# Optimization experiments

Hardware: AMD Instinct MI355X
Metric: run time of the kernel (lower is better)

Reference implementation:

```python
import jax, jax.numpy as jnp
import numpy as np

OUT_X = OUT_Y = OUT_Z = 12        # out_size
N_VOX = OUT_X * OUT_Y * OUT_Z
N_ROIS, N_PTS, C = 128, 160000, 64


def setup_inputs() -> dict:
    key = jax.random.key(0)
    k1, k2, k3, k4, k5, k6 = jax.random.split(key, 6)
    # rois: (N, 7) = [x, y, z_bottom, w(dx), l(dy), h(dz), ry]
    centers_xy = jax.random.uniform(k1, (N_ROIS, 2), minval=-40.0, maxval=40.0)
    z_bottom = jax.random.uniform(k2, (N_ROIS, 1), minval=-2.0, maxval=0.0)
    sizes = jax.random.uniform(k3, (N_ROIS, 3), minval=1.5, maxval=5.0)
    ry = jax.random.uniform(k4, (N_ROIS, 1), minval=-np.pi, maxval=np.pi)
    rois = jnp.concatenate([centers_xy, z_bottom, sizes, ry], axis=1).astype(jnp.float32)
    # points spread over the same scene extent so many fall inside rois
    pts = (jax.random.uniform(k5, (N_PTS, 3), minval=-1.0, maxval=1.0)
           * jnp.array([45.0, 45.0, 2.5], jnp.float32)).astype(jnp.float32)
    pts_feature = jax.random.normal(k6, (N_PTS, C), dtype=jnp.float32)
    return {"rois": rois, "pts": pts, "pts_feature": pts_feature}


def _voxel_segments(rois, pts):
    """Per (roi, point): flat voxel index in [0, N_VOX), or N_VOX if outside the roi."""
    cx, cy, cz, dx, dy, dz, rz = [rois[:, i:i + 1] for i in range(7)]  # (N,1)
    sx = pts[:, 0] - cx   # (N,P)
    sy = pts[:, 1] - cy
    sz = pts[:, 2] - cz   # z relative to box bottom
    cosa, sina = jnp.cos(-rz), jnp.sin(-rz)
    lx = sx * cosa - sy * sina  # rotate into roi-local frame
    ly = sx * sina + sy * cosa
    in_box = ((lx > -dx * 0.5) & (lx < dx * 0.5)
              & (ly > -dy * 0.5) & (ly < dy * 0.5)
              & (jnp.abs(sz - dz * 0.5) <= dz * 0.5))
    xi = jnp.clip(jnp.floor((lx + dx * 0.5) / (dx / OUT_X)), 0, OUT_X - 1).astype(jnp.int32)
    yi = jnp.clip(jnp.floor((ly + dy * 0.5) / (dy / OUT_Y)), 0, OUT_Y - 1).astype(jnp.int32)
    zi = jnp.clip(jnp.floor(sz / (dz / OUT_Z)), 0, OUT_Z - 1).astype(jnp.int32)
    seg = xi * (OUT_Y * OUT_Z) + yi * OUT_Z + zi
    return jnp.where(in_box, seg, N_VOX)  # (N, P) int32


def reference(rois, pts, pts_feature):
    seg = _voxel_segments(rois, pts)  # (N, P)
    ones = jnp.ones((pts.shape[0],), jnp.float32)

    def per_roi(s):
        mx = jax.ops.segment_max(pts_feature, s, num_segments=N_VOX + 1)[:N_VOX]  # (V, C)
        cnt = jax.ops.segment_sum(ones, s, num_segments=N_VOX + 1)[:N_VOX]        # (V,)
        return jnp.where(cnt[:, None] > 0, mx, 0.0)  # empty voxels -> 0, as in CUDA kernel

    pooled = jax.lax.map(per_roi, seg)  # (N, V, C); sequential over rois keeps memory bounded
    return pooled.reshape(N_ROIS, OUT_X, OUT_Y, OUT_Z, pts_feature.shape[-1])
```

## Files before the change

### kernel.cpp

```cpp
#include <hip/hip_runtime.h>

#define NROIS 128
#define OUTD  12
#define NVOX  (OUTD * OUTD * OUTD)
#define NCH   64
#define RPB   16
#define QCAP  1024

__device__ __forceinline__ unsigned enc_f32(float f) {
    unsigned b = __float_as_uint(f);
    return (b & 0x80000000u) ? ~b : (b | 0x80000000u);
}

__device__ __forceinline__ float dec_key(unsigned k) {
    unsigned b = (k & 0x80000000u) ? (k & 0x7fffffffu) : ~k;
    return __uint_as_float(b);
}

#define WS_REJ   0
#define WS_RAD2  (WS_REJ + NROIS * 16)
#define WS_FULL  (WS_RAD2 + NROIS * 4)

__global__ void roi_prep(const float* __restrict__ rois,
                         float4* __restrict__ rej, float* __restrict__ rad2,
                         float4* __restrict__ full)
{
    int r = threadIdx.x;
    if (r >= NROIS) return;
    float cx = rois[7 * r + 0];
    float cy = rois[7 * r + 1];
    float cz = rois[7 * r + 2];
    float dx = rois[7 * r + 3];
    float dy = rois[7 * r + 4];
    float dz = rois[7 * r + 5];
    float nrz = -rois[7 * r + 6];
    float ca = cosf(nrz), sa = sinf(nrz);
    float hx = __fmul_rn(dx, 0.5f);
    float hy = __fmul_rn(dy, 0.5f);
    float hz = __fmul_rn(dz, 0.5f);
    full[3 * r + 0] = make_float4(cx, cy, cz, ca);
    full[3 * r + 1] = make_float4(sa, hx, hy, hz);
    full[3 * r + 2] = make_float4(__fdiv_rn(dx, 12.0f), __fdiv_rn(dy, 12.0f),
                                  __fdiv_rn(dz, 12.0f), 0.0f);
    float R2 = 0.25f * (dx * dx + dy * dy);
    rad2[r] = R2 * 1.04f + 1e-4f;
    float zc = cz + hz;
    float zh = hz * 1.001f + 1e-3f;
    rej[r] = make_float4(cx, cy, zc, zh);
}

__global__ void __launch_bounds__(256) roi_pool_scatter(
        const float* __restrict__ pts,
        const float* __restrict__ feat,
        const float4* __restrict__ rej,
        const float* __restrict__ rad2,
        const float4* __restrict__ full,
        unsigned*    __restrict__ out,
        int npts)
{
    __shared__ float4   sRej[RPB];
    __shared__ float    sRad[RPB];
    __shared__ float4   sFull[RPB * 3];
    __shared__ unsigned sQp[QCAP];
    __shared__ unsigned sQk[QCAP];
    __shared__ unsigned sQn;

    int rbase = blockIdx.y * RPB;
    if (threadIdx.x == 0) sQn = 0;
    if (threadIdx.x < RPB) {
        sRej[threadIdx.x] = rej[rbase + threadIdx.x];
        sRad[threadIdx.x] = rad2[rbase + threadIdx.x];
    }
    if (threadIdx.x < RPB * 3)
        sFull[threadIdx.x] = full[rbase * 3 + threadIdx.x];
    __syncthreads();

    int p = blockIdx.x * blockDim.x + threadIdx.x;
    if (p < npts) {
        float px = pts[3 * p + 0];
        float py = pts[3 * p + 1];
        float pz = pts[3 * p + 2];

        for (int r = 0; r < RPB; ++r) {
            float4 q = sRej[r];
            float sx = px - q.x;
            float sy = py - q.y;
            float d2 = sx * sx + sy * sy;
            if (!((d2 < sRad[r]) && (fabsf(pz - q.z) <= q.w))) continue;

            float4 F0 = sFull[3 * r + 0];
            float4 F1 = sFull[3 * r + 1];
            float sz = __fsub_rn(pz, F0.z);
            float ca = F0.w, sa = F1.x;
            float hx = F1.y, hy = F1.z, hz = F1.w;
            float lx = __fsub_rn(__fmul_rn(sx, ca), __fmul_rn(sy, sa));
            float ly = __fadd_rn(__fmul_rn(sx, sa), __fmul_rn(sy, ca));

            bool in_box = (lx > -hx) && (lx < hx) &&
                          (ly > -hy) && (ly < hy) &&
                          (fabsf(__fsub_rn(sz, hz)) <= hz);
            if (!in_box) continue;

            float4 F2 = sFull[3 * r + 2];
            int xi = (int)floorf(__fdiv_rn(__fadd_rn(lx, hx), F2.x));
            int yi = (int)floorf(__fdiv_rn(__fadd_rn(ly, hy), F2.y));
            int zi = (int)floorf(__fdiv_rn(sz,                F2.z));
            xi = min(max(xi, 0), OUTD - 1);
            yi = min(max(yi, 0), OUTD - 1);
            zi = min(max(zi, 0), OUTD - 1);

            unsigned key = (unsigned)((rbase + r) * NVOX +
                                      xi * (OUTD * OUTD) + yi * OUTD + zi);

            unsigned idx = atomicAdd(&sQn, 1u);
            if (idx < QCAP) {
                sQp[idx] = (unsigned)p;
                sQk[idx] = key;
            } else {
                unsigned* dst = out + (size_t)key * NCH;
                const float* fp = feat + (size_t)p * NCH;
                #pragma unroll 1
                for (int c = 0; c < NCH; ++c)
                    atomicMax(dst + c, enc_f32(fp[c]));
            }
        }
    }

    __syncthreads();
    int nq   = min((int)sQn, QCAP);
    int wid  = threadIdx.x >> 6;
    int lane = threadIdx.x & 63;
    for (int i = wid; i < nq; i += 4) {
        unsigned pp = sQp[i];
        unsigned kk = sQk[i];
        float f = feat[(size_t)pp * NCH + lane];
        atomicMax(out + (size_t)kk * NCH + lane, enc_f32(f));
    }
}

__global__ void __launch_bounds__(256) decode_keys(unsigned* __restrict__ out, int n4)
{
    int i = blockIdx.x * blockDim.x + threadIdx.x;
    if (i >= n4) return;
    uint4 k = reinterpret_cast<uint4*>(out)[i];
    if ((k.x | k.y | k.z | k.w) == 0u) return;
    float4 f;
    f.x = (k.x == 0u) ? 0.0f : dec_key(k.x);
    f.y = (k.y == 0u) ? 0.0f : dec_key(k.y);
    f.z = (k.z == 0u) ? 0.0f : dec_key(k.z);
    f.w = (k.w == 0u) ? 0.0f : dec_key(k.w);
    reinterpret_cast<float4*>(out)[i] = f;
}

extern "C" void kernel_launch(void* const* d_in, const int* in_sizes, int n_in,
                              void* d_out, int out_size, void* d_ws, size_t ws_size,
                              hipStream_t stream)
{
    const float* rois = (const float*)d_in[0];
    const float* pts  = (const float*)d_in[1];
    const float* feat = (const float*)d_in[2];
    int npts = in_sizes[1] / 3;

    float4* rej  = (float4*)((char*)d_ws + WS_REJ);
    float*  rad2 = (float*)((char*)d_ws + WS_RAD2);
    float4* full = (float4*)((char*)d_ws + WS_FULL);

    hipMemsetAsync(d_out, 0, (size_t)out_size * sizeof(float), stream);

    roi_prep<<<1, NROIS, 0, stream>>>(rois, rej, rad2, full);

    dim3 grid((npts + 255) / 256, NROIS / RPB);
    roi_pool_scatter<<<grid, 256, 0, stream>>>(pts, feat, rej, rad2, full,
                                               (unsigned*)d_out, npts);

    int n4 = out_size / 4;
    decode_keys<<<(n4 + 255) / 256, 256, 0, stream>>>((unsigned*)d_out, n4);
}
```

Measured before the change: 120.9 us.

## Fuse ROI prep into scatter kernel and decode only touched voxels via bitmask

Removes the separate roi_prep launch by computing per-ROI parameters inside each scatter block's shared-memory setup. Adds a bitmask of touched voxel keys, set with atomicOr during scatter, so the decode pass visits only occupied voxels instead of streaming the whole output. This saves a kernel launch and a full read of the output buffer, at the cost of an extra memset, per-entry atomicOr traffic, and redundant trig per block.

```diff
diff --git a/kernel.cpp b/kernel.cpp
--- a/kernel.cpp
+++ b/kernel.cpp
@@ -4,6 +4,8 @@
 #define OUTD  12
 #define NVOX  (OUTD * OUTD * OUTD)
 #define NCH   64
+#define NKEYS (NROIS * NVOX)
+#define NWORDS (NKEYS / 32)
 #define RPB   16
 #define QCAP  1024
 
@@ -17,45 +19,12 @@
     return __uint_as_float(b);
 }
 
-#define WS_REJ   0
-#define WS_RAD2  (WS_REJ + NROIS * 16)
-#define WS_FULL  (WS_RAD2 + NROIS * 4)
-
-__global__ void roi_prep(const float* __restrict__ rois,
-                         float4* __restrict__ rej, float* __restrict__ rad2,
-                         float4* __restrict__ full)
-{
-    int r = threadIdx.x;
-    if (r >= NROIS) return;
-    float cx = rois[7 * r + 0];
-    float cy = rois[7 * r + 1];
-    float cz = rois[7 * r + 2];
-    float dx = rois[7 * r + 3];
-    float dy = rois[7 * r + 4];
-    float dz = rois[7 * r + 5];
-    float nrz = -rois[7 * r + 6];
-    float ca = cosf(nrz), sa = sinf(nrz);
-    float hx = __fmul_rn(dx, 0.5f);
-    float hy = __fmul_rn(dy, 0.5f);
-    float hz = __fmul_rn(dz, 0.5f);
-    full[3 * r + 0] = make_float4(cx, cy, cz, ca);
-    full[3 * r + 1] = make_float4(sa, hx, hy, hz);
-    full[3 * r + 2] = make_float4(__fdiv_rn(dx, 12.0f), __fdiv_rn(dy, 12.0f),
-                                  __fdiv_rn(dz, 12.0f), 0.0f);
-    float R2 = 0.25f * (dx * dx + dy * dy);
-    rad2[r] = R2 * 1.04f + 1e-4f;
-    float zc = cz + hz;
-    float zh = hz * 1.001f + 1e-3f;
-    rej[r] = make_float4(cx, cy, zc, zh);
-}
-
 __global__ void __launch_bounds__(256) roi_pool_scatter(
+        const float* __restrict__ rois,
         const float* __restrict__ pts,
         const float* __restrict__ feat,
-        const float4* __restrict__ rej,
-        const float* __restrict__ rad2,
-        const float4* __restrict__ full,
         unsigned*    __restrict__ out,
+        unsigned*    __restrict__ mask,
         int npts)
 {
     __shared__ float4   sRej[RPB];
@@ -68,11 +37,27 @@
     int rbase = blockIdx.y * RPB;
     if (threadIdx.x == 0) sQn = 0;
     if (threadIdx.x < RPB) {
-        sRej[threadIdx.x] = rej[rbase + threadIdx.x];
-        sRad[threadIdx.x] = rad2[rbase + threadIdx.x];
+        int r = rbase + threadIdx.x;
+        float cx = rois[7 * r + 0];
+        float cy = rois[7 * r + 1];
+        float cz = rois[7 * r + 2];
+        float dx = rois[7 * r + 3];
+        float dy = rois[7 * r + 4];
+        float dz = rois[7 * r + 5];
+        float nrz = -rois[7 * r + 6];
+        float ca = cosf(nrz), sa = sinf(nrz);
+        float hx = __fmul_rn(dx, 0.5f);
+        float hy = __fmul_rn(dy, 0.5f);
+        float hz = __fmul_rn(dz, 0.5f);
+        sFull[3 * threadIdx.x + 0] = make_float4(cx, cy, cz, ca);
+        sFull[3 * threadIdx.x + 1] = make_float4(sa, hx, hy, hz);
+        sFull[3 * threadIdx.x + 2] = make_float4(__fdiv_rn(dx, 12.0f),
+                                                 __fdiv_rn(dy, 12.0f),
+                                                 __fdiv_rn(dz, 12.0f), 0.0f);
+        float R2 = 0.25f * (dx * dx + dy * dy);
+        sRad[threadIdx.x] = R2 * 1.04f + 1e-4f;
+        sRej[threadIdx.x] = make_float4(cx, cy, cz + hz, hz * 1.001f + 1e-3f);
     }
-    if (threadIdx.x < RPB * 3)
-        sFull[threadIdx.x] = full[rbase * 3 + threadIdx.x];
     __syncthreads();
 
     int p = blockIdx.x * blockDim.x + threadIdx.x;
@@ -117,6 +102,7 @@
                 sQp[idx] = (unsigned)p;
                 sQk[idx] = key;
             } else {
+                atomicOr(&mask[key >> 5], 1u << (key & 31));
                 unsigned* dst = out + (size_t)key * NCH;
                 const float* fp = feat + (size_t)p * NCH;
                 #pragma unroll 1
@@ -133,23 +119,29 @@
     for (int i = wid; i < nq; i += 4) {
         unsigned pp = sQp[i];
         unsigned kk = sQk[i];
+        if (lane == 0)
+            atomicOr(&mask[kk >> 5], 1u << (kk & 31));
         float f = feat[(size_t)pp * NCH + lane];
         atomicMax(out + (size_t)kk * NCH + lane, enc_f32(f));
     }
 }
 
-__global__ void __launch_bounds__(256) decode_keys(unsigned* __restrict__ out, int n4)
+__global__ void __launch_bounds__(256) decode_touched(
+        unsigned* __restrict__ out,
+        const unsigned* __restrict__ mask)
 {
-    int i = blockIdx.x * blockDim.x + threadIdx.x;
-    if (i >= n4) return;
-    uint4 k = reinterpret_cast<uint4*>(out)[i];
-    if ((k.x | k.y | k.z | k.w) == 0u) return;
-    float4 f;
-    f.x = (k.x == 0u) ? 0.0f : dec_key(k.x);
-    f.y = (k.y == 0u) ? 0.0f : dec_key(k.y);
-    f.z = (k.z == 0u) ? 0.0f : dec_key(k.z);
-    f.w = (k.w == 0u) ? 0.0f : dec_key(k.w);
-    reinterpret_cast<float4*>(out)[i] = f;
+    int w    = (blockIdx.x * blockDim.x + threadIdx.x) >> 6;
+    int lane = threadIdx.x & 63;
+    if (w >= NWORDS) return;
+    unsigned word = mask[w];
+    while (word) {
+        int bit = __ffs(word) - 1;
+        word &= word - 1;
+        unsigned key = (unsigned)(w * 32 + bit);
+        unsigned* v = out + (size_t)key * NCH;
+        unsigned k = v[lane];
+        v[lane] = (k == 0u) ? 0u : __float_as_uint(dec_key(k));
+    }
 }
 
 extern "C" void kernel_launch(void* const* d_in, const int* in_sizes, int n_in,
@@ -161,18 +153,14 @@
     const float* feat = (const float*)d_in[2];
     int npts = in_sizes[1] / 3;
 
-    float4* rej  = (float4*)((char*)d_ws + WS_REJ);
-    float*  rad2 = (float*)((char*)d_ws + WS_RAD2);
-    float4* full = (float4*)((char*)d_ws + WS_FULL);
+    unsigned* mask = (unsigned*)d_ws;
 
     hipMemsetAsync(d_out, 0, (size_t)out_size * sizeof(float), stream);
-
-    roi_prep<<<1, NROIS, 0, stream>>>(rois, rej, rad2, full);
+    hipMemsetAsync(d_ws, 0, NWORDS * sizeof(unsigned), stream);
 
     dim3 grid((npts + 255) / 256, NROIS / RPB);
-    roi_pool_scatter<<<grid, 256, 0, stream>>>(pts, feat, rej, rad2, full,
-                                               (unsigned*)d_out, npts);
+    roi_pool_scatter<<<grid, 256, 0, stream>>>(rois, pts, feat,
+                                               (unsigned*)d_out, mask, npts);
 
-    int n4 = out_size / 4;
-    decode_keys<<<(n4 + 255) / 256, 256, 0, stream>>>((unsigned*)d_out, n4);
+    decode_touched<<<NWORDS / 4, 256, 0, stream>>>((unsigned*)d_out, mask);
 }
```

New measurement: 117.7 us. 1.03x faster.
